# Performance work log

Measured on AMD Instinct MI355X. Metric: run time of the kernel, lower is better.

## Reference

```python
import jax, jax.numpy as jnp
import numpy as np

B, T, E, H, V, D, C = 16384, 128, 32, 128, 30001, 128, 3


def setup_inputs() -> dict:
    key = jax.random.key(0)
    ks = jax.random.split(key, 8)
    tokens = jax.random.randint(ks[0], (B, T), 0, V, dtype=jnp.int32)
    emb = jax.random.normal(ks[1], (V, E), jnp.float32) * 0.05
    W = jax.random.normal(ks[2], (E, 3 * H), jnp.float32) * (1.0 / np.sqrt(E))
    U = jax.random.normal(ks[3], (H, 3 * H), jnp.float32) * (1.0 / np.sqrt(H))
    b = jnp.zeros((2, 3 * H), jnp.float32)  # [input_bias, recurrent_bias] (reset_after=True)
    W1 = jax.random.normal(ks[4], (H, D), jnp.float32) * (1.0 / np.sqrt(H))
    b1 = jnp.zeros((D,), jnp.float32)
    Wout = jax.random.normal(ks[5], (D, C), jnp.float32) * (1.0 / np.sqrt(D))
    bout = jnp.zeros((C,), jnp.float32)
    return {"tokens": tokens, "emb": emb, "W": W, "U": U, "b": b,
            "W1": W1, "b1": b1, "Wout": Wout, "bout": bout}


def _gru_masked(x, mask, W, U, b):
    # x: [B,T,E], mask: [B,T] bool. Keras GRU defaults: reset_after=True,
    # activation=tanh, recurrent_activation=sigmoid. Masked steps freeze state.
    xp = jnp.einsum('bte,eg->btg', x, W) + b[0]  # precompute input projections [B,T,3H]

    def step(h, inp):
        xg, m = inp                      # xg: [B,3H], m: [B]
        rec = h @ U + b[1]               # [B,3H]
        z = jax.nn.sigmoid(xg[:, :H] + rec[:, :H])
        r = jax.nn.sigmoid(xg[:, H:2 * H] + rec[:, H:2 * H])
        hh = jnp.tanh(xg[:, 2 * H:] + r * rec[:, 2 * H:])
        h_new = z * h + (1.0 - z) * hh
        h = jnp.where(m[:, None], h_new, h)
        return h, None

    h0 = jnp.zeros((x.shape[0], H), x.dtype)
    h, _ = jax.lax.scan(step, h0, (jnp.swapaxes(xp, 0, 1), jnp.swapaxes(mask, 0, 1)))
    return h


def reference(tokens, emb, W, U, b, W1, b1, Wout, bout):
    x = emb[tokens]                      # [B,T,E] embedding lookup
    mask = tokens != 0                   # mask_zero=True
    h = _gru_masked(x, mask, W, U, b)    # [B,H]
    d = h @ W1 + b1
    d = d * jax.nn.sigmoid(d)            # swish
    logits = d @ Wout + bout
    return jax.nn.softmax(logits, axis=-1)
```

## Files before the change

### kernel.cpp

```cpp
#include <hip/hip_runtime.h>
#include <hip/hip_fp16.h>

#define B_ 16384
#define T_ 128
#define E_ 32
#define H_ 128
#define G3_ 384
#define V_ 30001
#define D_ 128
#define C_ 3

#define LOG2E 1.44269504088896340736f

typedef _Float16 f16;
typedef f16 f16x4 __attribute__((ext_vector_type(4)));
typedef f16 f16x8 __attribute__((ext_vector_type(8)));
typedef float f32x4 __attribute__((ext_vector_type(4)));
typedef unsigned int u32;
typedef u32 u32x4 __attribute__((ext_vector_type(4)));

#define H0_OFF   0
#define H1_OFF   4096
#define TOK_OFF  8192
#define DBUF_OFF 16448
#define LDS_TOTAL 24896

__device__ __forceinline__ float frcp_(float x)  { return __builtin_amdgcn_rcpf(x); }
__device__ __forceinline__ float fexp2_(float x) { return __builtin_amdgcn_exp2f(x); }

#define BAR_LGKM() asm volatile("s_waitcnt lgkmcnt(0)\n\ts_barrier" ::: "memory")

#define K1_ROWS 8
__global__ __launch_bounds__(384) void embw_kernel(
    const float* __restrict__ emb,
    const float* __restrict__ W,
    const float* __restrict__ b,
    f16* __restrict__ embW)
{
    __shared__ float sW[E_][G3_];
    __shared__ float sE[K1_ROWS][E_];
    const int g = threadIdx.x;
    #pragma unroll
    for (int e = 0; e < E_; ++e) sW[e][g] = W[e * G3_ + g];
    const int v0 = blockIdx.x * K1_ROWS;
    for (int idx = g; idx < K1_ROWS * E_; idx += 384) {
        int rr = idx >> 5, ee = idx & 31;
        int v = v0 + rr;
        sE[rr][ee] = (v < V_) ? emb[v * E_ + ee] : 0.f;
    }
    __syncthreads();
    const float bg = b[g] + ((g < 256) ? b[G3_ + g] : 0.f);
    const int c = g & 127, slot = g >> 7;
    const float sc = (slot == 2) ? (2.f * LOG2E) : (-LOG2E);
    #pragma unroll
    for (int rr = 0; rr < K1_ROWS; ++rr) {
        int v = v0 + rr;
        if (v >= V_) break;
        float acc = bg;
        #pragma unroll
        for (int e = 0; e < E_; ++e) acc = fmaf(sE[rr][e], sW[e][g], acc);
        embW[(size_t)v * 512 + c * 4 + slot] = (f16)(acc * sc);
    }
}

__global__ __launch_bounds__(512, 4) void gru_mfma_kernel(
    const int*   __restrict__ tokens,
    const f16*   __restrict__ embW,
    const float* __restrict__ U,
    const float* __restrict__ b,
    const float* __restrict__ W1,
    const float* __restrict__ b1,
    const float* __restrict__ Wout,
    const float* __restrict__ bout,
    float* __restrict__ out)
{
    __shared__ char lds[LDS_TOTAL];
    const int tid = threadIdx.x;
    const int w   = tid >> 6;
    const int l   = tid & 63;
    const int cl  = l & 15;
    const int q   = l >> 4;
    const int R0  = blockIdx.x * 16;
    const int col = w * 16 + cl;

    for (int idx = tid; idx < 16 * T_; idx += 512) {
        int r = idx >> 7, t = idx & 127;
        u32 tok = (u32)tokens[(size_t)(R0 + r) * T_ + t];
        *(u32*)(&lds[TOK_OFF + t * 64 + r * 4]) = tok * 1024u;
    }
    if (tid < 16)
        *(u32*)(&lds[TOK_OFF + 128 * 64 + tid * 4]) = 0u;
    for (int idx = tid; idx < 1024; idx += 512)
        ((float*)(lds + H0_OFF))[idx] = 0.f;

    f16x8 Bf[3][4];
    #pragma unroll
    for (int gt = 0; gt < 3; ++gt) {
        const float sc = (gt == 2) ? (2.f * LOG2E) : (-LOG2E);
        const int n = gt * 128 + col;
        #pragma unroll
        for (int kt = 0; kt < 4; ++kt) {
            const int k0 = kt * 32 + q * 8;
            f16x8 fr;
            #pragma unroll
            for (int j = 0; j < 8; ++j)
                fr[j] = (f16)(U[(size_t)(k0 + j) * G3_ + n] * sc);
            Bf[gt][kt] = fr;
        }
    }

    const float bhs = 2.f * LOG2E * b[G3_ + 256 + col];
    const f32x4 bh4 = {bhs, bhs, bhs, bhs};

    float hreg[4];
    #pragma unroll
    for (int i = 0; i < 4; ++i) hreg[i] = 0.f;

    __syncthreads();

    const char* embWb = (const char*)embW;
    const int col8 = col * 8;

    u32x4 offc = *(const u32x4*)(&lds[TOK_OFF + q * 16]);
    f16x4 xvc[4];
    #pragma unroll
    for (int i = 0; i < 4; ++i)
        xvc[i] = *(const f16x4*)(embWb + offc[i] + col8);

    int cur = 0;
    for (int t = 0; t < T_; ++t) {
        const char* hb = lds + (cur ? H1_OFF : H0_OFF);
        char*       hn = lds + (cur ? H0_OFF : H1_OFF);

        const u32x4 offn = *(const u32x4*)(&lds[TOK_OFF + (t + 1) * 64 + q * 16]);
        f16x4 xvn[4];
        #pragma unroll
        for (int i = 0; i < 4; ++i)
            xvn[i] = *(const f16x4*)(embWb + offn[i] + col8);

        f16x8 af[4];
        #pragma unroll
        for (int kt = 0; kt < 4; ++kt) {
            const int chunk = (kt * 64 + q * 16) ^ ((cl & 7) << 4);
            af[kt] = *(const f16x8*)(hb + cl * 256 + chunk);
        }
        f32x4 xz4, xr4;
        #pragma unroll
        for (int i = 0; i < 4; ++i) {
            xz4[i] = (float)xvc[i][0];
            xr4[i] = (float)xvc[i][1];
        }
        f32x4 accz = __builtin_amdgcn_mfma_f32_16x16x32_f16(af[0], Bf[0][0], xz4, 0, 0, 0);
        f32x4 accr = __builtin_amdgcn_mfma_f32_16x16x32_f16(af[0], Bf[1][0], xr4, 0, 0, 0);
        f32x4 acch = __builtin_amdgcn_mfma_f32_16x16x32_f16(af[0], Bf[2][0], bh4, 0, 0, 0);
        accz = __builtin_amdgcn_mfma_f32_16x16x32_f16(af[1], Bf[0][1], accz, 0, 0, 0);
        accr = __builtin_amdgcn_mfma_f32_16x16x32_f16(af[1], Bf[1][1], accr, 0, 0, 0);
        acch = __builtin_amdgcn_mfma_f32_16x16x32_f16(af[1], Bf[2][1], acch, 0, 0, 0);
        accz = __builtin_amdgcn_mfma_f32_16x16x32_f16(af[2], Bf[0][2], accz, 0, 0, 0);
        accr = __builtin_amdgcn_mfma_f32_16x16x32_f16(af[2], Bf[1][2], accr, 0, 0, 0);
        acch = __builtin_amdgcn_mfma_f32_16x16x32_f16(af[2], Bf[2][2], acch, 0, 0, 0);
        accz = __builtin_amdgcn_mfma_f32_16x16x32_f16(af[3], Bf[0][3], accz, 0, 0, 0);
        accr = __builtin_amdgcn_mfma_f32_16x16x32_f16(af[3], Bf[1][3], accr, 0, 0, 0);
        acch = __builtin_amdgcn_mfma_f32_16x16x32_f16(af[3], Bf[2][3], acch, 0, 0, 0);

        #pragma unroll
        for (int i = 0; i < 4; ++i) {
            const float ez = fexp2_(accz[i]);
            const float er = fexp2_(accr[i]);
            const float pz = 1.f + ez;
            const float pr = 1.f + er;
            const float inv = frcp_(pz * pr);
            const float z  = pr * inv;
            const float r  = pz * inv;
            const float hh = fmaf(-2.f, frcp_(1.f + fexp2_(fmaf(r, acch[i], (float)xvc[i][2]))), 1.f);
            const float hv = hreg[i];
            float nv = fmaf(z, hv - hh, hh);
            nv = (offc[i] != 0u) ? nv : hv;
            hreg[i] = nv;
            const int row = 4 * q + i;
            *(f16*)(hn + row * 256 + ((col * 2) ^ ((row & 7) << 4))) = (f16)nv;
        }
        BAR_LGKM();
        cur ^= 1;
        offc = offn;
        #pragma unroll
        for (int i = 0; i < 4; ++i) xvc[i] = xvn[i];
    }

    {
        f16x8 Wf[4];
        #pragma unroll
        for (int kt = 0; kt < 4; ++kt) {
            const int k0 = kt * 32 + q * 8;
            f16x8 fr;
            #pragma unroll
            for (int j = 0; j < 8; ++j)
                fr[j] = (f16)W1[(size_t)(k0 + j) * D_ + col];
            Wf[kt] = fr;
        }
        const char* hb = lds + H0_OFF;
        const float bd = b1[col];
        f32x4 dacc = {bd, bd, bd, bd};
        #pragma unroll
        for (int kt = 0; kt < 4; ++kt) {
            const int chunk = (kt * 64 + q * 16) ^ ((cl & 7) << 4);
            const f16x8 af = *(const f16x8*)(hb + cl * 256 + chunk);
            dacc = __builtin_amdgcn_mfma_f32_16x16x32_f16(af, Wf[kt], dacc, 0, 0, 0);
        }
        #pragma unroll
        for (int i = 0; i < 4; ++i) {
            const float v = dacc[i];
            const float sw = v * frcp_(1.f + fexp2_(-LOG2E * v));
            *(float*)(&lds[DBUF_OFF + (4 * q + i) * 528 + col * 4]) = sw;
        }
    }
    __syncthreads();

    if (w == 0 && l < 48) {
        const int row = l & 15, ci = l >> 4;
        float acc = bout[ci];
        #pragma unroll 4
        for (int k = 0; k < D_; ++k)
            acc = fmaf(*(const float*)(&lds[DBUF_OFF + row * 528 + k * 4]),
                       Wout[k * 3 + ci], acc);
        const float v0 = __shfl(acc, row);
        const float v1 = __shfl(acc, row + 16);
        const float v2 = __shfl(acc, row + 32);
        const float mx = fmaxf(v0, fmaxf(v1, v2));
        const float e0 = fexp2_(LOG2E * (v0 - mx));
        const float e1 = fexp2_(LOG2E * (v1 - mx));
        const float e2 = fexp2_(LOG2E * (v2 - mx));
        const float inv = frcp_(e0 + e1 + e2);
        const float mine = (ci == 0) ? e0 : (ci == 1) ? e1 : e2;
        out[(size_t)(R0 + row) * 3 + ci] = mine * inv;
    }
}

extern "C" void kernel_launch(void* const* d_in, const int* in_sizes, int n_in,
                              void* d_out, int out_size, void* d_ws, size_t ws_size,
                              hipStream_t stream) {
    (void)in_sizes; (void)n_in; (void)out_size; (void)ws_size;
    const int*   tokens = (const int*)d_in[0];
    const float* emb    = (const float*)d_in[1];
    const float* W      = (const float*)d_in[2];
    const float* U      = (const float*)d_in[3];
    const float* b      = (const float*)d_in[4];
    const float* W1     = (const float*)d_in[5];
    const float* b1     = (const float*)d_in[6];
    const float* Wout   = (const float*)d_in[7];
    const float* bout   = (const float*)d_in[8];
    float* out  = (float*)d_out;
    f16*   embW = (f16*)d_ws;

    hipLaunchKernelGGL(embw_kernel, dim3((V_ + K1_ROWS - 1) / K1_ROWS), dim3(384), 0, stream,
                       emb, W, b, embW);
    hipLaunchKernelGGL(gru_mfma_kernel, dim3(B_ / 16), dim3(512), 0, stream,
                       tokens, embW, U, b, W1, b1, Wout, bout, out);
}
```

Before: 365.9 us.

## Precompute exp2 of input gates in table, unroll recurrence by two, raise MFMA priority

The embedding-projection table now stores exp2 of the scaled input-gate pre-activations. In the recurrence the input contribution becomes a multiply after exp2 of the recurrent part instead of being fed as the MFMA accumulator, which drops the per-step f16-to-f32 conversions into the accumulator. The time loop is manually unrolled by two with fixed H0/H1 buffers, removing the buffer select and the register copies. s_setprio is raised around the MFMA chain. Storing exponentials in f16 risks overflow or precision loss for large pre-activations.

```diff
diff --git a/kernel.cpp b/kernel.cpp
--- a/kernel.cpp
+++ b/kernel.cpp
@@ -59,7 +59,7 @@
         float acc = bg;
         #pragma unroll
         for (int e = 0; e < E_; ++e) acc = fmaf(sE[rr][e], sW[e][g], acc);
-        embW[(size_t)v * 512 + c * 4 + slot] = (f16)(acc * sc);
+        embW[(size_t)v * 512 + c * 4 + slot] = (f16)fexp2_(acc * sc);
     }
 }
 
@@ -111,6 +111,7 @@
 
     const float bhs = 2.f * LOG2E * b[G3_ + 256 + col];
     const f32x4 bh4 = {bhs, bhs, bhs, bhs};
+    const f32x4 zero4 = {0.f, 0.f, 0.f, 0.f};
 
     float hreg[4];
     #pragma unroll
@@ -121,38 +122,17 @@
     const char* embWb = (const char*)embW;
     const int col8 = col * 8;
 
-    u32x4 offc = *(const u32x4*)(&lds[TOK_OFF + q * 16]);
-    f16x4 xvc[4];
-    #pragma unroll
-    for (int i = 0; i < 4; ++i)
-        xvc[i] = *(const f16x4*)(embWb + offc[i] + col8);
-
-    int cur = 0;
-    for (int t = 0; t < T_; ++t) {
-        const char* hb = lds + (cur ? H1_OFF : H0_OFF);
-        char*       hn = lds + (cur ? H0_OFF : H1_OFF);
-
-        const u32x4 offn = *(const u32x4*)(&lds[TOK_OFF + (t + 1) * 64 + q * 16]);
-        f16x4 xvn[4];
-        #pragma unroll
-        for (int i = 0; i < 4; ++i)
-            xvn[i] = *(const f16x4*)(embWb + offn[i] + col8);
-
+    auto step = [&](const char* hb, char* hn, const u32x4& off, const f16x4* xv) {
         f16x8 af[4];
         #pragma unroll
         for (int kt = 0; kt < 4; ++kt) {
             const int chunk = (kt * 64 + q * 16) ^ ((cl & 7) << 4);
             af[kt] = *(const f16x8*)(hb + cl * 256 + chunk);
         }
-        f32x4 xz4, xr4;
-        #pragma unroll
-        for (int i = 0; i < 4; ++i) {
-            xz4[i] = (float)xvc[i][0];
-            xr4[i] = (float)xvc[i][1];
-        }
-        f32x4 accz = __builtin_amdgcn_mfma_f32_16x16x32_f16(af[0], Bf[0][0], xz4, 0, 0, 0);
-        f32x4 accr = __builtin_amdgcn_mfma_f32_16x16x32_f16(af[0], Bf[1][0], xr4, 0, 0, 0);
-        f32x4 acch = __builtin_amdgcn_mfma_f32_16x16x32_f16(af[0], Bf[2][0], bh4, 0, 0, 0);
+        __builtin_amdgcn_s_setprio(1);
+        f32x4 accz = __builtin_amdgcn_mfma_f32_16x16x32_f16(af[0], Bf[0][0], zero4, 0, 0, 0);
+        f32x4 accr = __builtin_amdgcn_mfma_f32_16x16x32_f16(af[0], Bf[1][0], zero4, 0, 0, 0);
+        f32x4 acch = __builtin_amdgcn_mfma_f32_16x16x32_f16(af[0], Bf[2][0], bh4,  0, 0, 0);
         accz = __builtin_amdgcn_mfma_f32_16x16x32_f16(af[1], Bf[0][1], accz, 0, 0, 0);
         accr = __builtin_amdgcn_mfma_f32_16x16x32_f16(af[1], Bf[1][1], accr, 0, 0, 0);
         acch = __builtin_amdgcn_mfma_f32_16x16x32_f16(af[1], Bf[2][1], acch, 0, 0, 0);
@@ -162,29 +142,48 @@
         accz = __builtin_amdgcn_mfma_f32_16x16x32_f16(af[3], Bf[0][3], accz, 0, 0, 0);
         accr = __builtin_amdgcn_mfma_f32_16x16x32_f16(af[3], Bf[1][3], accr, 0, 0, 0);
         acch = __builtin_amdgcn_mfma_f32_16x16x32_f16(af[3], Bf[2][3], acch, 0, 0, 0);
+        __builtin_amdgcn_s_setprio(0);
 
         #pragma unroll
         for (int i = 0; i < 4; ++i) {
-            const float ez = fexp2_(accz[i]);
-            const float er = fexp2_(accr[i]);
+            const float ez = fexp2_(accz[i]) * (float)xv[i][0];
+            const float er = fexp2_(accr[i]) * (float)xv[i][1];
             const float pz = 1.f + ez;
             const float pr = 1.f + er;
             const float inv = frcp_(pz * pr);
             const float z  = pr * inv;
             const float r  = pz * inv;
-            const float hh = fmaf(-2.f, frcp_(1.f + fexp2_(fmaf(r, acch[i], (float)xvc[i][2]))), 1.f);
+            const float eh = fexp2_(r * acch[i]) * (float)xv[i][2];
+            const float hh = fmaf(-2.f, frcp_(1.f + eh), 1.f);
             const float hv = hreg[i];
             float nv = fmaf(z, hv - hh, hh);
-            nv = (offc[i] != 0u) ? nv : hv;
+            nv = (off[i] != 0u) ? nv : hv;
             hreg[i] = nv;
             const int row = 4 * q + i;
             *(f16*)(hn + row * 256 + ((col * 2) ^ ((row & 7) << 4))) = (f16)nv;
         }
         BAR_LGKM();
-        cur ^= 1;
-        offc = offn;
-        #pragma unroll
-        for (int i = 0; i < 4; ++i) xvc[i] = xvn[i];
+    };
+
+    u32x4 offA = *(const u32x4*)(&lds[TOK_OFF + q * 16]);
+    f16x4 xvA[4];
+    #pragma unroll
+    for (int i = 0; i < 4; ++i)
+        xvA[i] = *(const f16x4*)(embWb + offA[i] + col8);
+
+    for (int t = 0; t < T_; t += 2) {
+        const u32x4 offB = *(const u32x4*)(&lds[TOK_OFF + (t + 1) * 64 + q * 16]);
+        f16x4 xvB[4];
+        #pragma unroll
+        for (int i = 0; i < 4; ++i)
+            xvB[i] = *(const f16x4*)(embWb + offB[i] + col8);
+        step(lds + H0_OFF, lds + H1_OFF, offA, xvA);
+
+        offA = *(const u32x4*)(&lds[TOK_OFF + (t + 2) * 64 + q * 16]);
+        #pragma unroll
+        for (int i = 0; i < 4; ++i)
+            xvA[i] = *(const f16x4*)(embWb + offA[i] + col8);
+        step(lds + H1_OFF, lds + H0_OFF, offB, xvB);
     }
 
     {
```

Result: faster. 356.0 us (-2.7%).
